# Kernel optimization log

Hardware: AMD Instinct MI355X
Metric: run time of the kernel (lower is better)

The kernel has to match this reference:

```python
import jax, jax.numpy as jnp
import numpy as np

N = 50000      # nodes
E = 800000     # edges
D = 64         # input_dim = hidden_dim = output_dim
ED = 16        # edge_attr dim
L = 4          # total GATConv layers (2 per GAT block)
G = 64         # number of graphs in the batch vector
NEG_SLOPE = 0.2


def setup_inputs() -> dict:
    key = jax.random.key(0)
    ks = jax.random.split(key, 12)
    s = 0.1
    x = jax.random.normal(ks[0], (N, D), jnp.float32)
    edge_index = jax.random.randint(ks[1], (2, E), 0, N, jnp.int32)
    edge_attr = jax.random.normal(ks[2], (E, ED), jnp.float32)
    batch = jnp.sort(jax.random.randint(ks[3], (N,), 0, G, jnp.int32))
    return {
        "x": x,
        "edge_index": edge_index,
        "edge_attr": edge_attr,
        "batch": batch,
        # stacked per-layer GATConv params (all layers are D->D)
        "W": jax.random.normal(ks[4], (L, D, D), jnp.float32) * s,
        "a_src": jax.random.normal(ks[5], (L, D), jnp.float32) * s,
        "a_dst": jax.random.normal(ks[6], (L, D), jnp.float32) * s,
        "We": jax.random.normal(ks[7], (L, ED, D), jnp.float32) * s,
        "a_e": jax.random.normal(ks[8], (L, D), jnp.float32) * s,
        "b": jnp.zeros((L, D), jnp.float32),
        "Wfc": jax.random.normal(ks[9], (D, 2048), jnp.float32) * s,
        "bfc": jnp.zeros((2048,), jnp.float32),
    }


def _gat_conv(h, src, dst, edge_attr, W, a_s, a_d, We, a_e, b):
    # single-head GATConv with edge features (PyG semantics, flow src->dst)
    hw = h @ W                                      # [N, D]
    el = (edge_attr @ We) @ a_e                     # [E]
    score = jax.nn.leaky_relu(
        (hw @ a_s)[src] + (hw @ a_d)[dst] + el, NEG_SLOPE)  # [E]
    # softmax over incoming edges of each dst node
    m = jax.ops.segment_max(score, dst, num_segments=N)      # [N]
    p = jnp.exp(score - m[dst])                               # [E]
    denom = jax.ops.segment_sum(p, dst, num_segments=N)      # [N]
    alpha = p / denom[dst]                                    # [E]
    out = jax.ops.segment_sum(alpha[:, None] * hw[src], dst, num_segments=N)
    return out + b


def reference(x, edge_index, edge_attr, batch, W, a_src, a_dst, We, a_e, b, Wfc, bfc):
    src, dst = edge_index[0], edge_index[1]
    h = x
    for l in range(L):
        h = _gat_conv(h, src, dst, edge_attr,
                      W[l], a_src[l], a_dst[l], We[l], a_e[l], b[l])
        if l < L - 1:  # relu inside blocks and between the two GAT blocks
            h = jax.nn.relu(h)
    # global_mean_pool over batch vector
    counts = jax.ops.segment_sum(jnp.ones((N,), h.dtype), batch, num_segments=G)
    pooled = jax.ops.segment_sum(h, batch, num_segments=G) / jnp.maximum(counts, 1.0)[:, None]
    out = pooled @ Wfc + bfc                        # [G, 2048]
    return out[None]                                # stacked over list -> [1, G, 2048]
```

## Files before the change

### kernel.cpp

```cpp
#include <hip/hip_runtime.h>
#include <hip/hip_bf16.h>

#define NN 50000
#define EE 800000
#define DD 64
#define LL 4
#define GG 64
#define PJ 16
#define NXCD 8
#define DRANGE (NN / NXCD)

__global__ void k_ce(const float* __restrict__ We, const float* __restrict__ a_e,
                     float* __restrict__ ce) {
    int t = threadIdx.x;
    int l = t >> 4, k = t & 15;
    float acc = 0.f;
    for (int j = 0; j < 64; ++j)
        acc += We[l * 1024 + k * 64 + j] * a_e[l * 64 + j];
    ce[t] = acc;
}

__global__ __launch_bounds__(256) void k_el(const float* __restrict__ ea,
                                            const float* __restrict__ ce,
                                            float* __restrict__ el_all, int ne) {
    __shared__ float sce[64];
    if (threadIdx.x < 64) sce[threadIdx.x] = ce[threadIdx.x];
    __syncthreads();
    int e = blockIdx.x * 256 + threadIdx.x;
    if (e >= ne) return;
    const float4* p4 = reinterpret_cast<const float4*>(ea + (size_t)e * 16);
    float v[16];
    float4 q;
    q = p4[0]; v[0] = q.x; v[1] = q.y; v[2] = q.z; v[3] = q.w;
    q = p4[1]; v[4] = q.x; v[5] = q.y; v[6] = q.z; v[7] = q.w;
    q = p4[2]; v[8] = q.x; v[9] = q.y; v[10] = q.z; v[11] = q.w;
    q = p4[3]; v[12] = q.x; v[13] = q.y; v[14] = q.z; v[15] = q.w;
    float o[4];
#pragma unroll
    for (int l = 0; l < 4; ++l) {
        float a = 0.f;
#pragma unroll
        for (int k = 0; k < 16; ++k) a = fmaf(v[k], sce[l * 16 + k], a);
        o[l] = a;
    }
    reinterpret_cast<float4*>(el_all)[e] = make_float4(o[0], o[1], o[2], o[3]);
}

__global__ __launch_bounds__(256) void k_hist(const int* __restrict__ dst,
                                              int* __restrict__ counts, int ne) {
    int r = blockIdx.x;
    int e = blockIdx.y * 256 + threadIdx.x;
    if (e >= ne) return;
    int d = dst[e];
    int rlo = r * DRANGE;
    if (d < rlo || d >= rlo + DRANGE) return;
    atomicAdd(&counts[d], 1);
}

__global__ void k_scan1(const int* __restrict__ counts, int* __restrict__ bsum, int n) {
    __shared__ int s[256];
    int i = blockIdx.x * 256 + threadIdx.x;
    s[threadIdx.x] = (i < n) ? counts[i] : 0;
    __syncthreads();
    for (int off = 128; off; off >>= 1) {
        if (threadIdx.x < off) s[threadIdx.x] += s[threadIdx.x + off];
        __syncthreads();
    }
    if (threadIdx.x == 0) bsum[blockIdx.x] = s[0];
}

__global__ void k_scan2(int* __restrict__ bsum, int nb) {
    __shared__ int s[256];
    int t = threadIdx.x;
    int v = (t < nb) ? bsum[t] : 0;
    s[t] = v;
    __syncthreads();
    for (int off = 1; off < 256; off <<= 1) {
        int x = (t >= off) ? s[t - off] : 0;
        __syncthreads();
        s[t] += x;
        __syncthreads();
    }
    if (t < nb) bsum[t] = s[t] - v;
}

__global__ void k_scan3(const int* __restrict__ counts, const int* __restrict__ bsum,
                        int* __restrict__ row_ptr, int n) {
    __shared__ int s[256];
    int t = threadIdx.x;
    int i = blockIdx.x * 256 + t;
    int v = (i < n) ? counts[i] : 0;
    s[t] = v;
    __syncthreads();
    for (int off = 1; off < 256; off <<= 1) {
        int x = (t >= off) ? s[t - off] : 0;
        __syncthreads();
        s[t] += x;
        __syncthreads();
    }
    if (i < n) row_ptr[i] = s[t] - v + bsum[blockIdx.x];
}

__global__ __launch_bounds__(256) void k_fill(const int* __restrict__ dst,
                                              const int* __restrict__ row_ptr,
                                              int* __restrict__ cursor,
                                              int* __restrict__ csr_eid, int ne) {
    int r = blockIdx.x;
    int e = blockIdx.y * 256 + threadIdx.x;
    if (e >= ne) return;
    int d = dst[e];
    int rlo = r * DRANGE;
    if (d < rlo || d >= rlo + DRANGE) return;
    int pos = row_ptr[d] + atomicAdd(&cursor[d], 1);
    csr_eid[pos] = e;
}

__global__ __launch_bounds__(256) void k_sortperm(int* __restrict__ csr_eid,
                                                  const int* __restrict__ e_src,
                                                  const int* __restrict__ row_ptr,
                                                  const int* __restrict__ counts,
                                                  const float4* __restrict__ el_all,
                                                  int* __restrict__ csr_src,
                                                  float* __restrict__ e0, float* __restrict__ e1,
                                                  float* __restrict__ e2, float* __restrict__ e3,
                                                  int n) {
    int wid = threadIdx.x >> 6, lane = threadIdx.x & 63;
    int nd = blockIdx.x * 4 + wid;
    if (nd >= n) return;
    int s = row_ptr[nd], d = counts[nd];
    if (d == 0) return;
    if (d <= 64) {
        int eid = 0x7FFFFFFF;
        if (lane < d) eid = csr_eid[s + lane];
        int rank = 0;
        for (int j = 0; j < d; ++j) {
            int ej = __shfl(eid, j, 64);
            rank += (ej < eid) ? 1 : 0;
        }
        if (lane < d) {
            int sr = e_src[eid];
            float4 ev = el_all[eid];
            csr_src[s + rank] = sr;
            e0[s + rank] = ev.x; e1[s + rank] = ev.y;
            e2[s + rank] = ev.z; e3[s + rank] = ev.w;
        }
    } else if (lane == 0) {
        for (int i = 1; i < d; ++i) {
            int key = csr_eid[s + i];
            int j = i - 1;
            while (j >= 0 && csr_eid[s + j] > key) {
                csr_eid[s + j + 1] = csr_eid[s + j];
                --j;
            }
            csr_eid[s + j + 1] = key;
        }
        for (int i = 0; i < d; ++i) {
            int eid = csr_eid[s + i];
            float4 ev = el_all[eid];
            csr_src[s + i] = e_src[eid];
            e0[s + i] = ev.x; e1[s + i] = ev.y; e2[s + i] = ev.z; e3[s + i] = ev.w;
        }
    }
}

__global__ __launch_bounds__(256) void k_gemm(const float* __restrict__ h,
                                              const float* __restrict__ W,
                                              const float* __restrict__ a_s,
                                              const float* __restrict__ a_d,
                                              float* __restrict__ hw,
                                              float* __restrict__ ssrc,
                                              float* __restrict__ sdst, int n) {
    __shared__ float sHT[64 * 68];
    __shared__ float sW[64 * 64];
    int t = threadIdx.x;
    int nbase = blockIdx.x * 64;
    int nrem = n - nbase;
    const float4* W4 = (const float4*)W;
    float4* sW4 = (float4*)sW;
#pragma unroll
    for (int p = 0; p < 4; ++p) sW4[t + p * 256] = W4[t + p * 256];
#pragma unroll
    for (int p = 0; p < 4; ++p) {
        int idx = t + p * 256;
        int node = idx >> 4, d4 = idx & 15;
        float4 v = make_float4(0.f, 0.f, 0.f, 0.f);
        if (node < nrem) v = ((const float4*)(h + (size_t)(nbase + node) * 64))[d4];
        sHT[(d4 * 4 + 0) * 68 + node] = v.x;
        sHT[(d4 * 4 + 1) * 68 + node] = v.y;
        sHT[(d4 * 4 + 2) * 68 + node] = v.z;
        sHT[(d4 * 4 + 3) * 68 + node] = v.w;
    }
    __syncthreads();
    int nr = (t >> 4) * 4;
    int nc = (t & 15) * 4;
    float a0[4], a1[4], a2[4], a3[4];
#pragma unroll
    for (int j = 0; j < 4; ++j) { a0[j] = 0.f; a1[j] = 0.f; a2[j] = 0.f; a3[j] = 0.f; }
    for (int k = 0; k < 64; ++k) {
        float4 hv = *(const float4*)&sHT[k * 68 + nr];
        float4 wv = *(const float4*)&sW[k * 64 + nc];
        a0[0] = fmaf(hv.x, wv.x, a0[0]); a0[1] = fmaf(hv.x, wv.y, a0[1]);
        a0[2] = fmaf(hv.x, wv.z, a0[2]); a0[3] = fmaf(hv.x, wv.w, a0[3]);
        a1[0] = fmaf(hv.y, wv.x, a1[0]); a1[1] = fmaf(hv.y, wv.y, a1[1]);
        a1[2] = fmaf(hv.y, wv.z, a1[2]); a1[3] = fmaf(hv.y, wv.w, a1[3]);
        a2[0] = fmaf(hv.z, wv.x, a2[0]); a2[1] = fmaf(hv.z, wv.y, a2[1]);
        a2[2] = fmaf(hv.z, wv.z, a2[2]); a2[3] = fmaf(hv.z, wv.w, a2[3]);
        a3[0] = fmaf(hv.w, wv.x, a3[0]); a3[1] = fmaf(hv.w, wv.y, a3[1]);
        a3[2] = fmaf(hv.w, wv.z, a3[2]); a3[3] = fmaf(hv.w, wv.w, a3[3]);
    }
    if (nr + 0 < nrem) ((float4*)(hw + (size_t)(nbase + nr + 0) * 64))[t & 15] =
        make_float4(a0[0], a0[1], a0[2], a0[3]);
    if (nr + 1 < nrem) ((float4*)(hw + (size_t)(nbase + nr + 1) * 64))[t & 15] =
        make_float4(a1[0], a1[1], a1[2], a1[3]);
    if (nr + 2 < nrem) ((float4*)(hw + (size_t)(nbase + nr + 2) * 64))[t & 15] =
        make_float4(a2[0], a2[1], a2[2], a2[3]);
    if (nr + 3 < nrem) ((float4*)(hw + (size_t)(nbase + nr + 3) * 64))[t & 15] =
        make_float4(a3[0], a3[1], a3[2], a3[3]);
    float as0 = a_s[nc], as1 = a_s[nc + 1], as2 = a_s[nc + 2], as3 = a_s[nc + 3];
    float ad0 = a_d[nc], ad1 = a_d[nc + 1], ad2 = a_d[nc + 2], ad3 = a_d[nc + 3];
    float ts0 = fmaf(a0[3], as3, fmaf(a0[2], as2, fmaf(a0[1], as1, a0[0] * as0)));
    float ts1 = fmaf(a1[3], as3, fmaf(a1[2], as2, fmaf(a1[1], as1, a1[0] * as0)));
    float ts2 = fmaf(a2[3], as3, fmaf(a2[2], as2, fmaf(a2[1], as1, a2[0] * as0)));
    float ts3 = fmaf(a3[3], as3, fmaf(a3[2], as2, fmaf(a3[1], as1, a3[0] * as0)));
    float td0 = fmaf(a0[3], ad3, fmaf(a0[2], ad2, fmaf(a0[1], ad1, a0[0] * ad0)));
    float td1 = fmaf(a1[3], ad3, fmaf(a1[2], ad2, fmaf(a1[1], ad1, a1[0] * ad0)));
    float td2 = fmaf(a2[3], ad3, fmaf(a2[2], ad2, fmaf(a2[1], ad1, a2[0] * ad0)));
    float td3 = fmaf(a3[3], ad3, fmaf(a3[2], ad2, fmaf(a3[1], ad1, a3[0] * ad0)));
#pragma unroll
    for (int off = 1; off < 16; off <<= 1) {
        ts0 += __shfl_xor(ts0, off, 64); ts1 += __shfl_xor(ts1, off, 64);
        ts2 += __shfl_xor(ts2, off, 64); ts3 += __shfl_xor(ts3, off, 64);
        td0 += __shfl_xor(td0, off, 64); td1 += __shfl_xor(td1, off, 64);
        td2 += __shfl_xor(td2, off, 64); td3 += __shfl_xor(td3, off, 64);
    }
    if ((t & 15) == 0) {
        if (nr + 0 < nrem) { ssrc[nbase + nr + 0] = ts0; sdst[nbase + nr + 0] = td0; }
        if (nr + 1 < nrem) { ssrc[nbase + nr + 1] = ts1; sdst[nbase + nr + 1] = td1; }
        if (nr + 2 < nrem) { ssrc[nbase + nr + 2] = ts2; sdst[nbase + nr + 2] = td2; }
        if (nr + 3 < nrem) { ssrc[nbase + nr + 3] = ts3; sdst[nbase + nr + 3] = td3; }
    }
}

__global__ __launch_bounds__(256) void k_row(const float* __restrict__ hw,
                                             const float* __restrict__ ssrc,
                                             const float* __restrict__ sdstA,
                                             const int* __restrict__ csr_src,
                                             const float* __restrict__ elpL,
                                             const int* __restrict__ row_ptr,
                                             const int* __restrict__ counts,
                                             const float* __restrict__ bias,
                                             int relu_flag, float* __restrict__ hout, int n) {
    int wid = threadIdx.x >> 6, lane = threadIdx.x & 63;
    int nd = blockIdx.x * 4 + wid;
    if (nd >= n) return;
    int start = row_ptr[nd], deg = counts[nd];
    if (deg == 0) {
        float outv = bias[lane];
        if (relu_flag) outv = fmaxf(outv, 0.f);
        hout[(size_t)nd * 64 + lane] = outv;
        return;
    }
    if (deg <= 64) {
        float sdn = sdstA[nd];
        int p = start + lane;
        int s_l = 0;
        float sc = -INFINITY;
        if (lane < deg) {
            s_l = csr_src[p];
            sc = ssrc[s_l] + sdn + elpL[p];
            sc = sc > 0.f ? sc : 0.2f * sc;
        }
        float mx = sc;
#pragma unroll
        for (int off = 32; off; off >>= 1) mx = fmaxf(mx, __shfl_xor(mx, off, 64));
        float pe = (lane < deg) ? __expf(sc - mx) : 0.f;
        float dsum = pe;
#pragma unroll
        for (int off = 32; off; off >>= 1) dsum += __shfl_xor(dsum, off, 64);
        const float* hwL = hw + lane;
        float acc = 0.f;
        int t0 = __shfl(s_l, 0, 64), t1 = __shfl(s_l, 1, 64);
        int t2 = __shfl(s_l, 2, 64), t3 = __shfl(s_l, 3, 64);
        int t4 = __shfl(s_l, 4, 64), t5 = __shfl(s_l, 5, 64);
        int t6 = __shfl(s_l, 6, 64), t7 = __shfl(s_l, 7, 64);
        float v0 = hwL[(size_t)t0 * 64], v1 = hwL[(size_t)t1 * 64];
        float v2 = hwL[(size_t)t2 * 64], v3 = hwL[(size_t)t3 * 64];
        float v4 = hwL[(size_t)t4 * 64], v5 = hwL[(size_t)t5 * 64];
        float v6 = hwL[(size_t)t6 * 64], v7 = hwL[(size_t)t7 * 64];
        for (int i = 0; i < deg; i += 8) {
            float p0 = __shfl(pe, i, 64),     p1 = __shfl(pe, i + 1, 64);
            float p2 = __shfl(pe, i + 2, 64), p3 = __shfl(pe, i + 3, 64);
            float p4 = __shfl(pe, i + 4, 64), p5 = __shfl(pe, i + 5, 64);
            float p6 = __shfl(pe, i + 6, 64), p7 = __shfl(pe, i + 7, 64);
            int u0 = __shfl(s_l, (i + 8) & 63, 64),  u1 = __shfl(s_l, (i + 9) & 63, 64);
            int u2 = __shfl(s_l, (i + 10) & 63, 64), u3 = __shfl(s_l, (i + 11) & 63, 64);
            int u4 = __shfl(s_l, (i + 12) & 63, 64), u5 = __shfl(s_l, (i + 13) & 63, 64);
            int u6 = __shfl(s_l, (i + 14) & 63, 64), u7 = __shfl(s_l, (i + 15) & 63, 64);
            float w0 = v0, w1 = v1, w2 = v2, w3 = v3,
                  w4 = v4, w5 = v5, w6 = v6, w7 = v7;
            v0 = hwL[(size_t)u0 * 64]; v1 = hwL[(size_t)u1 * 64];
            v2 = hwL[(size_t)u2 * 64]; v3 = hwL[(size_t)u3 * 64];
            v4 = hwL[(size_t)u4 * 64]; v5 = hwL[(size_t)u5 * 64];
            v6 = hwL[(size_t)u6 * 64]; v7 = hwL[(size_t)u7 * 64];
            acc = fmaf(p0, w0, acc);
            acc = fmaf(p1, w1, acc);
            acc = fmaf(p2, w2, acc);
            acc = fmaf(p3, w3, acc);
            acc = fmaf(p4, w4, acc);
            acc = fmaf(p5, w5, acc);
            acc = fmaf(p6, w6, acc);
            acc = fmaf(p7, w7, acc);
        }
        float outv = acc / dsum + bias[lane];
        if (relu_flag) outv = fmaxf(outv, 0.f);
        hout[(size_t)nd * 64 + lane] = outv;
        return;
    }
    {
        float sdn = sdstA[nd];
        float mx = -INFINITY;
        for (int i = lane; i < deg; i += 64) {
            int p = start + i;
            float sc = ssrc[csr_src[p]] + sdn + elpL[p];
            sc = sc > 0.f ? sc : 0.2f * sc;
            mx = fmaxf(mx, sc);
        }
#pragma unroll
        for (int off = 32; off; off >>= 1) mx = fmaxf(mx, __shfl_xor(mx, off, 64));
        float dsum = 0.f;
        for (int i = lane; i < deg; i += 64) {
            int p = start + i;
            float sc = ssrc[csr_src[p]] + sdn + elpL[p];
            sc = sc > 0.f ? sc : 0.2f * sc;
            dsum += __expf(sc - mx);
        }
#pragma unroll
        for (int off = 32; off; off >>= 1) dsum += __shfl_xor(dsum, off, 64);
        float acc = 0.f;
        for (int i = 0; i < deg; ++i) {
            int p = start + i;
            int s = csr_src[p];
            float sc = ssrc[s] + sdn + elpL[p];
            sc = sc > 0.f ? sc : 0.2f * sc;
            float pex = __expf(sc - mx);
            acc = fmaf(pex, hw[(size_t)s * 64 + lane], acc);
        }
        float outv = acc / dsum + bias[lane];
        if (relu_flag) outv = fmaxf(outv, 0.f);
        hout[(size_t)nd * 64 + lane] = outv;
    }
}

__global__ __launch_bounds__(256) void k_pool_part(const float* __restrict__ h,
                                                   const int* __restrict__ batch,
                                                   float* __restrict__ partial, int n) {
    int g = blockIdx.y, j = blockIdx.x;
    int lo = 0, hi = n;
    while (lo < hi) { int mid = (lo + hi) >> 1; if (batch[mid] < g) lo = mid + 1; else hi = mid; }
    int start = lo;
    lo = start; hi = n;
    while (lo < hi) { int mid = (lo + hi) >> 1; if (batch[mid] < g + 1) lo = mid + 1; else hi = mid; }
    int end = lo;
    int cnt = end - start;
    int chunk = (cnt + PJ - 1) / PJ;
    int clo = start + j * chunk;
    int chi = min(clo + chunk, end);
    int lane = threadIdx.x & 63, q = threadIdx.x >> 6;
    float acc = 0.f;
    for (int nd = clo + q; nd < chi; nd += 4) acc += h[(size_t)nd * 64 + lane];
    __shared__ float s[4][64];
    s[q][lane] = acc;
    __syncthreads();
    if (threadIdx.x < 64) {
        float tot = s[0][threadIdx.x] + s[1][threadIdx.x] + s[2][threadIdx.x] + s[3][threadIdx.x];
        partial[((size_t)g * PJ + j) * 64 + threadIdx.x] = tot;
    }
}

__global__ __launch_bounds__(256) void k_fc(const float* __restrict__ partial,
                                            const int* __restrict__ batch,
                                            const float* __restrict__ Wfc,
                                            const float* __restrict__ bfc,
                                            float* __restrict__ out, int n) {
    int g = blockIdx.y;
    int c = blockIdx.x * 256 + threadIdx.x;
    __shared__ float sp[64];
    if (threadIdx.x < 64) {
        int d = threadIdx.x;
        float tot = 0.f;
#pragma unroll
        for (int j = 0; j < PJ; ++j) tot += partial[((size_t)g * PJ + j) * 64 + d];
        int lo = 0, hi = n;
        while (lo < hi) { int mid = (lo + hi) >> 1; if (batch[mid] < g) lo = mid + 1; else hi = mid; }
        int start = lo;
        lo = start; hi = n;
        while (lo < hi) { int mid = (lo + hi) >> 1; if (batch[mid] < g + 1) lo = mid + 1; else hi = mid; }
        int cnt = lo - start;
        sp[d] = tot / fmaxf((float)cnt, 1.0f);
    }
    __syncthreads();
    float acc = bfc[c];
#pragma unroll
    for (int k = 0; k < 64; ++k) acc = fmaf(sp[k], Wfc[k * 2048 + c], acc);
    out[(size_t)g * 2048 + c] = acc;
}

extern "C" void kernel_launch(void* const* d_in, const int* in_sizes, int n_in,
                              void* d_out, int out_size, void* d_ws, size_t ws_size,
                              hipStream_t stream) {
    const float* x = (const float*)d_in[0];
    const int* edge_index = (const int*)d_in[1];
    const float* edge_attr = (const float*)d_in[2];
    const int* batch = (const int*)d_in[3];
    const float* W = (const float*)d_in[4];
    const float* a_src = (const float*)d_in[5];
    const float* a_dst = (const float*)d_in[6];
    const float* We = (const float*)d_in[7];
    const float* a_e = (const float*)d_in[8];
    const float* b = (const float*)d_in[9];
    const float* Wfc = (const float*)d_in[10];
    const float* bfc = (const float*)d_in[11];
    float* out = (float*)d_out;

    char* ws = (char*)d_ws;
    size_t off = 0;
    auto alloc = [&](size_t bytes) {
        void* p = ws + off;
        off = (off + bytes + 255) & ~(size_t)255;
        return p;
    };
    float* h0      = (float*)alloc((size_t)NN * 64 * 4);
    float* h1      = (float*)alloc((size_t)NN * 64 * 4);
    float* hw      = (float*)alloc((size_t)NN * 64 * 4);
    float* ssrc    = (float*)alloc((size_t)NN * 4);
    float* sdst    = (float*)alloc((size_t)NN * 4);
    float* el_all  = (float*)alloc((size_t)EE * 16);
    float* elpT    = (float*)alloc((size_t)EE * 4 * 4);
    int*   csr_src = (int*)alloc((size_t)EE * 4);
    int*   csr_eid = (int*)alloc((size_t)EE * 4);
    int*   counts  = (int*)alloc((size_t)NN * 4);
    int*   row_ptr = (int*)alloc((size_t)NN * 4);
    int*   cursor  = (int*)alloc((size_t)NN * 4);
    int*   bsum    = (int*)alloc(256 * 4);
    float* ce      = (float*)alloc(64 * 4);
    float* partial = (float*)alloc((size_t)GG * PJ * 64 * 4);
    (void)ws_size; (void)in_sizes; (void)n_in; (void)out_size;

    const int* e_src = edge_index;
    const int* e_dst = edge_index + EE;
    const int EB = EE / 256;
    const int NB = (NN + 255) / 256;

    hipMemsetAsync(counts, 0, (size_t)NN * 4, stream);
    hipMemsetAsync(cursor, 0, (size_t)NN * 4, stream);

    k_ce<<<1, 64, 0, stream>>>(We, a_e, ce);
    k_el<<<EB, 256, 0, stream>>>(edge_attr, ce, el_all, EE);
    k_hist<<<dim3(NXCD, EB), 256, 0, stream>>>(e_dst, counts, EE);
    k_scan1<<<NB, 256, 0, stream>>>(counts, bsum, NN);
    k_scan2<<<1, 256, 0, stream>>>(bsum, NB);
    k_scan3<<<NB, 256, 0, stream>>>(counts, bsum, row_ptr, NN);
    k_fill<<<dim3(NXCD, EB), 256, 0, stream>>>(e_dst, row_ptr, cursor, csr_eid, EE);
    k_sortperm<<<(NN + 3) / 4, 256, 0, stream>>>(csr_eid, e_src, row_ptr, counts,
                                                 (const float4*)el_all, csr_src,
                                                 elpT, elpT + EE, elpT + 2 * (size_t)EE,
                                                 elpT + 3 * (size_t)EE, NN);

    const float* hin = x;
    float* hbufs[2] = {h0, h1};
    for (int l = 0; l < LL; ++l) {
        k_gemm<<<(NN + 63) / 64, 256, 0, stream>>>(hin, W + l * 4096, a_src + l * 64,
                                                   a_dst + l * 64, hw, ssrc, sdst, NN);
        float* hout = hbufs[l & 1];
        k_row<<<(NN + 3) / 4, 256, 0, stream>>>(hw, ssrc, sdst, csr_src,
                                                elpT + (size_t)l * EE, row_ptr, counts,
                                                b + l * 64, (l < LL - 1) ? 1 : 0, hout, NN);
        hin = hout;
    }
    k_pool_part<<<dim3(PJ, GG), 256, 0, stream>>>(hin, batch, partial, NN);
    k_fc<<<dim3(2048 / 256, GG), 256, 0, stream>>>(partial, batch, Wfc, bfc, out, NN);
}
```

Measured before the change: 356.1 us.

## Process two destination nodes per wavefront with half-wave float2 gather in k_row

The row aggregation kernel now assigns two destination nodes per 64-lane wavefront, each half-wave handling one node with float2 loads of hw rows and a software-pipelined 8-wide prefetch of neighbor features. Nodes with degree above 32 or zero fall back to the old per-node path. It also folds the tiny edge-coefficient kernel into k_el, which removes one launch at the cost of every block recomputing 64 dot products. The aim is to cut idle lanes for low-degree nodes (average degree about 16) and raise memory-level parallelism in the gather. The trade-off is branch divergence and extra shuffles, plus wasted loads when the two nodes' degrees differ.

```diff
diff --git a/kernel.cpp b/kernel.cpp
--- a/kernel.cpp
+++ b/kernel.cpp
@@ -10,21 +10,18 @@
 #define NXCD 8
 #define DRANGE (NN / NXCD)
 
-__global__ void k_ce(const float* __restrict__ We, const float* __restrict__ a_e,
-                     float* __restrict__ ce) {
-    int t = threadIdx.x;
-    int l = t >> 4, k = t & 15;
-    float acc = 0.f;
-    for (int j = 0; j < 64; ++j)
-        acc += We[l * 1024 + k * 64 + j] * a_e[l * 64 + j];
-    ce[t] = acc;
-}
-
 __global__ __launch_bounds__(256) void k_el(const float* __restrict__ ea,
-                                            const float* __restrict__ ce,
+                                            const float* __restrict__ We,
+                                            const float* __restrict__ a_e,
                                             float* __restrict__ el_all, int ne) {
     __shared__ float sce[64];
-    if (threadIdx.x < 64) sce[threadIdx.x] = ce[threadIdx.x];
+    if (threadIdx.x < 64) {
+        int l = threadIdx.x >> 4, k = threadIdx.x & 15;
+        float acc = 0.f;
+        for (int j = 0; j < 64; ++j)
+            acc += We[l * 1024 + k * 64 + j] * a_e[l * 64 + j];
+        sce[threadIdx.x] = acc;
+    }
     __syncthreads();
     int e = blockIdx.x * 256 + threadIdx.x;
     if (e >= ne) return;
@@ -241,18 +238,16 @@
     }
 }
 
-__global__ __launch_bounds__(256) void k_row(const float* __restrict__ hw,
-                                             const float* __restrict__ ssrc,
-                                             const float* __restrict__ sdstA,
-                                             const int* __restrict__ csr_src,
-                                             const float* __restrict__ elpL,
-                                             const int* __restrict__ row_ptr,
-                                             const int* __restrict__ counts,
-                                             const float* __restrict__ bias,
-                                             int relu_flag, float* __restrict__ hout, int n) {
-    int wid = threadIdx.x >> 6, lane = threadIdx.x & 63;
-    int nd = blockIdx.x * 4 + wid;
-    if (nd >= n) return;
+__device__ __forceinline__ void row_one_64(int nd, int lane,
+                                           const float* __restrict__ hw,
+                                           const float* __restrict__ ssrc,
+                                           const float* __restrict__ sdstA,
+                                           const int* __restrict__ csr_src,
+                                           const float* __restrict__ elpL,
+                                           const int* __restrict__ row_ptr,
+                                           const int* __restrict__ counts,
+                                           const float* __restrict__ bias,
+                                           int relu_flag, float* __restrict__ hout) {
     int start = row_ptr[nd], deg = counts[nd];
     if (deg == 0) {
         float outv = bias[lane];
@@ -351,6 +346,99 @@
     }
 }
 
+__global__ __launch_bounds__(256) void k_row(const float* __restrict__ hw,
+                                             const float* __restrict__ ssrc,
+                                             const float* __restrict__ sdstA,
+                                             const int* __restrict__ csr_src,
+                                             const float* __restrict__ elpL,
+                                             const int* __restrict__ row_ptr,
+                                             const int* __restrict__ counts,
+                                             const float* __restrict__ bias,
+                                             int relu_flag, float* __restrict__ hout, int n) {
+    int wid = threadIdx.x >> 6, lane = threadIdx.x & 63;
+    int nd0 = (blockIdx.x * 4 + wid) * 2;
+    if (nd0 >= n) return;
+    int g = lane >> 5, lg = lane & 31;
+    int ndg = nd0 + g;
+    bool v1ok = (nd0 + 1) < n;
+    int deg_g = (ndg < n) ? counts[ndg] : 0;
+    int deg0 = __shfl(deg_g, 0, 64);
+    int deg1 = __shfl(deg_g, 32, 64);
+    bool fast = v1ok && deg0 >= 1 && deg0 <= 32 && deg1 >= 1 && deg1 <= 32;
+    if (fast) {
+        int start = row_ptr[ndg];
+        float sdn = sdstA[ndg];
+        int p = start + lg;
+        int s_l = 0;
+        float sc = -INFINITY;
+        if (lg < deg_g) {
+            s_l = csr_src[p];
+            sc = ssrc[s_l] + sdn + elpL[p];
+            sc = sc > 0.f ? sc : 0.2f * sc;
+        }
+        float mx = sc;
+#pragma unroll
+        for (int off = 16; off; off >>= 1) mx = fmaxf(mx, __shfl_xor(mx, off, 64));
+        float pe = (lg < deg_g) ? __expf(sc - mx) : 0.f;
+        float dsum = pe;
+#pragma unroll
+        for (int off = 16; off; off >>= 1) dsum += __shfl_xor(dsum, off, 64);
+        int degmax = max(deg0, deg1);
+        int base = lane & 32;
+        const float2* hw2 = (const float2*)hw;
+        float2 acc = make_float2(0.f, 0.f);
+        int t0 = __shfl(s_l, base + 0, 64), t1 = __shfl(s_l, base + 1, 64);
+        int t2 = __shfl(s_l, base + 2, 64), t3 = __shfl(s_l, base + 3, 64);
+        int t4 = __shfl(s_l, base + 4, 64), t5 = __shfl(s_l, base + 5, 64);
+        int t6 = __shfl(s_l, base + 6, 64), t7 = __shfl(s_l, base + 7, 64);
+        float2 v0 = hw2[(size_t)t0 * 32 + lg], v1 = hw2[(size_t)t1 * 32 + lg];
+        float2 v2 = hw2[(size_t)t2 * 32 + lg], v3 = hw2[(size_t)t3 * 32 + lg];
+        float2 v4 = hw2[(size_t)t4 * 32 + lg], v5 = hw2[(size_t)t5 * 32 + lg];
+        float2 v6 = hw2[(size_t)t6 * 32 + lg], v7 = hw2[(size_t)t7 * 32 + lg];
+        for (int i = 0; i < degmax; i += 8) {
+            float p0 = __shfl(pe, base + i, 64),     p1 = __shfl(pe, base + i + 1, 64);
+            float p2 = __shfl(pe, base + i + 2, 64), p3 = __shfl(pe, base + i + 3, 64);
+            float p4 = __shfl(pe, base + i + 4, 64), p5 = __shfl(pe, base + i + 5, 64);
+            float p6 = __shfl(pe, base + i + 6, 64), p7 = __shfl(pe, base + i + 7, 64);
+            int u0 = __shfl(s_l, base + ((i + 8) & 31), 64);
+            int u1 = __shfl(s_l, base + ((i + 9) & 31), 64);
+            int u2 = __shfl(s_l, base + ((i + 10) & 31), 64);
+            int u3 = __shfl(s_l, base + ((i + 11) & 31), 64);
+            int u4 = __shfl(s_l, base + ((i + 12) & 31), 64);
+            int u5 = __shfl(s_l, base + ((i + 13) & 31), 64);
+            int u6 = __shfl(s_l, base + ((i + 14) & 31), 64);
+            int u7 = __shfl(s_l, base + ((i + 15) & 31), 64);
+            float2 w0 = v0, w1 = v1, w2 = v2, w3 = v3,
+                   w4 = v4, w5 = v5, w6 = v6, w7 = v7;
+            v0 = hw2[(size_t)u0 * 32 + lg]; v1 = hw2[(size_t)u1 * 32 + lg];
+            v2 = hw2[(size_t)u2 * 32 + lg]; v3 = hw2[(size_t)u3 * 32 + lg];
+            v4 = hw2[(size_t)u4 * 32 + lg]; v5 = hw2[(size_t)u5 * 32 + lg];
+            v6 = hw2[(size_t)u6 * 32 + lg]; v7 = hw2[(size_t)u7 * 32 + lg];
+            acc.x = fmaf(p0, w0.x, acc.x); acc.y = fmaf(p0, w0.y, acc.y);
+            acc.x = fmaf(p1, w1.x, acc.x); acc.y = fmaf(p1, w1.y, acc.y);
+            acc.x = fmaf(p2, w2.x, acc.x); acc.y = fmaf(p2, w2.y, acc.y);
+            acc.x = fmaf(p3, w3.x, acc.x); acc.y = fmaf(p3, w3.y, acc.y);
+            acc.x = fmaf(p4, w4.x, acc.x); acc.y = fmaf(p4, w4.y, acc.y);
+            acc.x = fmaf(p5, w5.x, acc.x); acc.y = fmaf(p5, w5.y, acc.y);
+            acc.x = fmaf(p6, w6.x, acc.x); acc.y = fmaf(p6, w6.y, acc.y);
+            acc.x = fmaf(p7, w7.x, acc.x); acc.y = fmaf(p7, w7.y, acc.y);
+        }
+        float2 bv = ((const float2*)bias)[lg];
+        float2 o;
+        o.x = acc.x / dsum + bv.x;
+        o.y = acc.y / dsum + bv.y;
+        if (relu_flag) { o.x = fmaxf(o.x, 0.f); o.y = fmaxf(o.y, 0.f); }
+        ((float2*)(hout + (size_t)ndg * 64))[lg] = o;
+        return;
+    }
+    for (int q = 0; q < 2; ++q) {
+        int nd = nd0 + q;
+        if (nd < n)
+            row_one_64(nd, lane, hw, ssrc, sdstA, csr_src, elpL, row_ptr, counts,
+                       bias, relu_flag, hout);
+    }
+}
+
 __global__ __launch_bounds__(256) void k_pool_part(const float* __restrict__ h,
                                                    const int* __restrict__ batch,
                                                    float* __restrict__ partial, int n) {
@@ -442,7 +530,6 @@
     int*   row_ptr = (int*)alloc((size_t)NN * 4);
     int*   cursor  = (int*)alloc((size_t)NN * 4);
     int*   bsum    = (int*)alloc(256 * 4);
-    float* ce      = (float*)alloc(64 * 4);
     float* partial = (float*)alloc((size_t)GG * PJ * 64 * 4);
     (void)ws_size; (void)in_sizes; (void)n_in; (void)out_size;
 
@@ -454,8 +541,7 @@
     hipMemsetAsync(counts, 0, (size_t)NN * 4, stream);
     hipMemsetAsync(cursor, 0, (size_t)NN * 4, stream);
 
-    k_ce<<<1, 64, 0, stream>>>(We, a_e, ce);
-    k_el<<<EB, 256, 0, stream>>>(edge_attr, ce, el_all, EE);
+    k_el<<<EB, 256, 0, stream>>>(edge_attr, We, a_e, el_all, EE);
     k_hist<<<dim3(NXCD, EB), 256, 0, stream>>>(e_dst, counts, EE);
     k_scan1<<<NB, 256, 0, stream>>>(counts, bsum, NN);
     k_scan2<<<1, 256, 0, stream>>>(bsum, NB);
@@ -472,7 +558,7 @@
         k_gemm<<<(NN + 63) / 64, 256, 0, stream>>>(hin, W + l * 4096, a_src + l * 64,
                                                    a_dst + l * 64, hw, ssrc, sdst, NN);
         float* hout = hbufs[l & 1];
-        k_row<<<(NN + 3) / 4, 256, 0, stream>>>(hw, ssrc, sdst, csr_src,
+        k_row<<<(NN + 7) / 8, 256, 0, stream>>>(hw, ssrc, sdst, csr_src,
                                                 elpT + (size_t)l * EE, row_ptr, counts,
                                                 b + l * 64, (l < LL - 1) ? 1 : 0, hout, NN);
         hin = hout;
```

After: 342.2 us. 3.9% less time.
